# Performance work log

Measured on AMD Instinct MI355X. Metric: run time of the kernel, lower is better.

## Reference

```python
import jax, jax.numpy as jnp
import numpy as np

H = 768        # bert hidden_size
HID = 512      # lstm_hidden
HALF = HID // 2
T = 20         # tagset_size
START, STOP = 18, 19
S = 16386      # input positions incl. CLS/SEP
NEG = -10000.0


def setup_inputs() -> dict:
    key = jax.random.key(0)
    ks = jax.random.split(key, 12)
    sc_x = 1.0
    x = jax.random.normal(ks[0], (1, S, H), dtype=jnp.float32)
    # PyTorch LSTM params (gate order i,f,g,o), one layer, bidirectional
    s_ih = 1.0 / np.sqrt(HALF)
    w_ih_f = jax.random.uniform(ks[1], (4 * HALF, H), jnp.float32, -s_ih, s_ih)
    w_hh_f = jax.random.uniform(ks[2], (4 * HALF, HALF), jnp.float32, -s_ih, s_ih)
    b_ih_f = jax.random.uniform(ks[3], (4 * HALF,), jnp.float32, -s_ih, s_ih)
    b_hh_f = jax.random.uniform(ks[4], (4 * HALF,), jnp.float32, -s_ih, s_ih)
    w_ih_b = jax.random.uniform(ks[5], (4 * HALF, H), jnp.float32, -s_ih, s_ih)
    w_hh_b = jax.random.uniform(ks[6], (4 * HALF, HALF), jnp.float32, -s_ih, s_ih)
    b_ih_b = jax.random.uniform(ks[7], (4 * HALF,), jnp.float32, -s_ih, s_ih)
    b_hh_b = jax.random.uniform(ks[8], (4 * HALF,), jnp.float32, -s_ih, s_ih)
    s_t = 1.0 / np.sqrt(HID)
    w_tag = jax.random.uniform(ks[9], (T, HID), jnp.float32, -s_t, s_t)
    b_tag = jax.random.uniform(ks[10], (T,), jnp.float32, -s_t, s_t)
    transitions = jax.random.normal(ks[11], (T, T), dtype=jnp.float32)
    transitions = transitions.at[START, :].set(NEG).at[:, STOP].set(NEG)
    return {
        "x": x,
        "w_ih_f": w_ih_f, "w_hh_f": w_hh_f, "b_ih_f": b_ih_f, "b_hh_f": b_hh_f,
        "w_ih_b": w_ih_b, "w_hh_b": w_hh_b, "b_ih_b": b_ih_b, "b_hh_b": b_hh_b,
        "w_tag": w_tag, "b_tag": b_tag, "transitions": transitions,
    }


def _lstm_one_step(xt, w_ih, b_ih, b_hh):
    # Original passes [1, N, H] to a batch_first=False LSTM => seq_len=1,
    # batch=N, zero initial state. So each token does ONE cell step:
    # h0=c0=0 => hh contribution is only b_hh.
    g = xt @ w_ih.T + b_ih + b_hh          # [N, 4*HALF]
    i, f, gg, o = jnp.split(g, 4, axis=-1)  # PyTorch gate order i,f,g,o
    c = jax.nn.sigmoid(i) * jnp.tanh(gg)    # f*c0 = 0
    return jax.nn.sigmoid(o) * jnp.tanh(c)  # [N, HALF]


def reference(x, w_ih_f, w_hh_f, b_ih_f, b_hh_f,
              w_ih_b, w_hh_b, b_ih_b, b_hh_b,
              w_tag, b_tag, transitions):
    tok = x[0, 1:-1, :]                     # narrow(1,1,S-2): drop CLS/SEP -> [N,H]
    h_f = _lstm_one_step(tok, w_ih_f, b_ih_f, b_hh_f)
    h_b = _lstm_one_step(tok, w_ih_b, b_ih_b, b_hh_b)
    enc = jnp.concatenate([h_f, h_b], axis=-1)   # [N, HID]
    feats = enc @ w_tag.T + b_tag                # [N, T] emission scores

    # ---- Viterbi decode (sequential DP over tokens) ----
    init = jnp.full((T,), NEG, dtype=feats.dtype).at[START].set(0.0)

    def vstep(fv, feat):
        scores = fv[None, :] + transitions       # [next_tag, prev_tag]
        bp = jnp.argmax(scores, axis=1)          # backpointers [T]
        fv_new = jnp.max(scores, axis=1) + feat
        return fv_new, bp

    fv, bps = jax.lax.scan(vstep, init, feats)   # bps: [N, T]
    terminal = fv + transitions[STOP]
    best = jnp.argmax(terminal)
    path_score = terminal[best]

    def btrack(b, bp):
        return bp[b], b                          # emit tag at time t, move to t-1

    _, best_path = jax.lax.scan(btrack, best, bps, reverse=True)  # [N] in time order
    return path_score, best_path
```

## Files before the change

kernel.cpp:

```cpp
#include <hip/hip_runtime.h>
#include <math.h>

#define HDIM 768
#define HIDD 512
#define NTOK 16384
#define NT 20
#define CHUNKS 128
#define CLEN 128

typedef unsigned short ushort_t;
typedef __attribute__((ext_vector_type(8))) short bf16x8;
typedef __attribute__((ext_vector_type(4))) float f32x4;

__device__ __forceinline__ float sigm(float x){ return 1.0f/(1.0f+expf(-x)); }

__device__ __forceinline__ ushort_t f2bf(float f){
    unsigned int u = __float_as_uint(f);
    unsigned int r = (u + 0x7fffu + ((u >> 16) & 1u)) >> 16;
    return (ushort_t)r;
}
__device__ __forceinline__ float bf2f(ushort_t b){
    return __uint_as_float(((unsigned int)b) << 16);
}

#define GLD16(gp, lp) __builtin_amdgcn_global_load_lds( \
    (const __attribute__((address_space(1))) void*)(gp), \
    (__attribute__((address_space(3))) void*)(lp), 16, 0, 0)

__global__ __launch_bounds__(256) void conv_kernel(
    const float* __restrict__ x,
    const float* __restrict__ wf, const float* __restrict__ wb,
    ushort_t* __restrict__ Ah, ushort_t* __restrict__ Al,
    ushort_t* __restrict__ Bh, ushort_t* __restrict__ Bl)
{
    const int bid = blockIdx.x;
    if (bid < 1152){
        int t = bid*256 + threadIdx.x;
        int n = t / 192, c4 = (t - n*192)*4;
        int dir = n / 768, nr = n - dir*768;
        int gate = nr >> 8, j = nr & 255;
        int wrow = j + ((gate==0)?0:((gate==1)?512:768));
        const float* src = dir ? wb : wf;
        const float4 v = *(const float4*)(src + (size_t)wrow*HDIM + c4);
        float f[4] = {v.x, v.y, v.z, v.w};
        ushort_t h[4], l[4];
        #pragma unroll
        for (int i=0;i<4;++i){
            h[i] = f2bf(f[i]);
            l[i] = f2bf(f[i] - bf2f(h[i]));
        }
        *(ushort4*)(Bh + (size_t)n*HDIM + c4) = make_ushort4(h[0],h[1],h[2],h[3]);
        *(ushort4*)(Bl + (size_t)n*HDIM + c4) = make_ushort4(l[0],l[1],l[2],l[3]);
    } else {
        int t = (bid-1152)*256 + threadIdx.x;
        int row = t / 192, c4 = (t - row*192)*4;
        const float4 v = *(const float4*)(x + (size_t)(row+1)*HDIM + c4);
        float f[4] = {v.x, v.y, v.z, v.w};
        ushort_t h[4], l[4];
        #pragma unroll
        for (int i=0;i<4;++i){
            h[i] = f2bf(f[i]);
            l[i] = f2bf(f[i] - bf2f(h[i]));
        }
        *(ushort4*)(Ah + (size_t)row*HDIM + c4) = make_ushort4(h[0],h[1],h[2],h[3]);
        *(ushort4*)(Al + (size_t)row*HDIM + c4) = make_ushort4(l[0],l[1],l[2],l[3]);
    }
}

__global__ __launch_bounds__(256, 4) void gemm_fused(
    const ushort_t* __restrict__ Ah, const ushort_t* __restrict__ Al,
    const ushort_t* __restrict__ Bh, const ushort_t* __restrict__ Bl,
    const float* __restrict__ bihf, const float* __restrict__ bhhf,
    const float* __restrict__ bihb, const float* __restrict__ bhhb,
    const float* __restrict__ wtag, float* __restrict__ featsp)
{
    __shared__ __align__(16) char smem[32768];
    ushort_t* As_h = (ushort_t*)smem;
    ushort_t* As_l = (ushort_t*)(smem + 4096);
    ushort_t* Bs_h = (ushort_t*)(smem + 8192);
    ushort_t* Bs_l = (ushort_t*)(smem + 16384);
    float* hbuf = (float*)smem;
    float* wts  = (float*)(smem + 16512);

    const int tid = threadIdx.x;
    const int bx = blockIdx.x;
    const int xcd = bx & 7, bidx = bx >> 3;
    const int q = bidx & 3, mt = (bidx >> 2)*8 + xcd;
    const int dir = q >> 1, j0 = (q & 1)*128;
    const int row0 = mt*64;
    const float* __restrict__ bih = dir ? bihb : bihf;
    const float* __restrict__ bhh = dir ? bhhb : bhhf;

    const int lane = tid & 63, wv = tid >> 6;
    const int wm = wv >> 1, wn = wv & 1;
    const int lm = lane & 15, lq = lane >> 4;
    const int wbase = (tid & 192) * 8;

    const int sr = tid >> 2;
    const int k8s = (tid & 3) ^ ((sr & 3) ^ ((sr >> 2) & 3));
    const size_t aoffe = (size_t)(row0 + sr)*HDIM + k8s*8;
    size_t boffe[2];
    #pragma unroll
    for (int g=0; g<2; ++g)
        boffe[g] = (size_t)(g*64 + sr)*HDIM + k8s*8;

    int aoff_lds[2], boff_lds[4];
    #pragma unroll
    for (int f=0; f<2; ++f){
        int m = wm*32 + f*16 + lm;
        int k8p = (lq ^ (m & 3) ^ ((m >> 2) & 3)) & 3;
        aoff_lds[f] = (m*4 + k8p)*8;
    }
    #pragma unroll
    for (int f=0; f<4; ++f){
        int n = wn*64 + f*16 + lm;
        int k8p = (lq ^ (n & 3) ^ ((n >> 2) & 3)) & 3;
        boff_lds[f] = (n*4 + k8p)*8;
    }

    int jcol[4];
    #pragma unroll
    for (int fn=0; fn<4; ++fn) jcol[fn] = j0 + wn*64 + fn*16 + lm;

    float held[2][4][4];
    f32x4 acc[2][4];

    #pragma unroll 1
    for (int p=0; p<3; ++p){
        const size_t bbase = (size_t)(dir*768 + p*256 + j0)*HDIM;

        #pragma unroll
        for (int fm=0; fm<2; ++fm)
            #pragma unroll
            for (int fn=0; fn<4; ++fn)
                acc[fm][fn] = (f32x4){0.f,0.f,0.f,0.f};

        #pragma unroll 1
        for (int kt=0; kt<24; ++kt){
            const int k0 = kt*32;
            GLD16(Ah + aoffe + k0,            &As_h[wbase]);
            GLD16(Al + aoffe + k0,            &As_l[wbase]);
            GLD16(Bh + bbase + boffe[0] + k0, &Bs_h[wbase]);
            GLD16(Bh + bbase + boffe[1] + k0, &Bs_h[2048 + wbase]);
            GLD16(Bl + bbase + boffe[0] + k0, &Bs_l[wbase]);
            GLD16(Bl + bbase + boffe[1] + k0, &Bs_l[2048 + wbase]);
            __syncthreads();
            bf16x8 afh[2], afl[2], bfh[4], bfl[4];
            #pragma unroll
            for (int f=0; f<2; ++f){
                afh[f] = *(const bf16x8*)&As_h[aoff_lds[f]];
                afl[f] = *(const bf16x8*)&As_l[aoff_lds[f]];
            }
            #pragma unroll
            for (int f=0; f<4; ++f){
                bfh[f] = *(const bf16x8*)&Bs_h[boff_lds[f]];
                bfl[f] = *(const bf16x8*)&Bs_l[boff_lds[f]];
            }
            #pragma unroll
            for (int fm=0; fm<2; ++fm)
                #pragma unroll
                for (int fn=0; fn<4; ++fn){
                    acc[fm][fn] = __builtin_amdgcn_mfma_f32_16x16x32_bf16(
                        afh[fm], bfh[fn], acc[fm][fn], 0, 0, 0);
                    acc[fm][fn] = __builtin_amdgcn_mfma_f32_16x16x32_bf16(
                        afl[fm], bfh[fn], acc[fm][fn], 0, 0, 0);
                    acc[fm][fn] = __builtin_amdgcn_mfma_f32_16x16x32_bf16(
                        afh[fm], bfl[fn], acc[fm][fn], 0, 0, 0);
                }
            __syncthreads();
        }

        const int gbase = (p==0) ? 0 : ((p==1) ? 512 : 768);
        float bias[4];
        #pragma unroll
        for (int fn=0; fn<4; ++fn)
            bias[fn] = bih[gbase + jcol[fn]] + bhh[gbase + jcol[fn]];

        if (p==0){
            #pragma unroll
            for (int fm=0; fm<2; ++fm)
                #pragma unroll
                for (int fn=0; fn<4; ++fn)
                    #pragma unroll
                    for (int r=0; r<4; ++r)
                        held[fm][fn][r] = sigm(acc[fm][fn][r] + bias[fn]);
        } else if (p==1){
            #pragma unroll
            for (int fm=0; fm<2; ++fm)
                #pragma unroll
                for (int fn=0; fn<4; ++fn)
                    #pragma unroll
                    for (int r=0; r<4; ++r)
                        held[fm][fn][r] *= tanhf(acc[fm][fn][r] + bias[fn]);
        } else {
            float hv[2][4][4];
            #pragma unroll
            for (int fm=0; fm<2; ++fm)
                #pragma unroll
                for (int fn=0; fn<4; ++fn)
                    #pragma unroll
                    for (int r=0; r<4; ++r)
                        hv[fm][fn][r] = sigm(acc[fm][fn][r] + bias[fn]) * tanhf(held[fm][fn][r]);

            for (int i2=tid; i2<NT*128; i2+=256){
                int t = i2 >> 7, j = i2 & 127;
                wts[i2] = wtag[t*HIDD + dir*256 + j0 + j];
            }
            float* fq = featsp + (size_t)q * (NTOK*NT);
            #pragma unroll 1
            for (int ph=0; ph<2; ++ph){
                __syncthreads();
                if (wm == ph){
                    #pragma unroll
                    for (int fm=0; fm<2; ++fm)
                        #pragma unroll
                        for (int fn=0; fn<4; ++fn)
                            #pragma unroll
                            for (int r=0; r<4; ++r){
                                int mloc = fm*16 + lq*4 + r;
                                int jloc = wn*64 + fn*16 + lm;
                                hbuf[mloc*129 + jloc] = hv[fm][fn][r];
                            }
                }
                __syncthreads();
                const int mrow = tid & 31, grp = tid >> 5;
                if (grp < 5){
                    const int tg0 = grp*4;
                    float s[4] = {0.f,0.f,0.f,0.f};
                    for (int j=0;j<128;++j){
                        float h = hbuf[mrow*129 + j];
                        #pragma unroll
                        for (int tt=0; tt<4; ++tt)
                            s[tt] = fmaf(h, wts[(tg0+tt)*128 + j], s[tt]);
                    }
                    const int mglob = row0 + ph*32 + mrow;
                    #pragma unroll
                    for (int tt=0; tt<4; ++tt)
                        fq[(size_t)mglob*NT + tg0 + tt] = s[tt];
                }
            }
        }
    }
}

__device__ __forceinline__ void load_fl(
    const float* __restrict__ featsp, const float* __restrict__ btg,
    float* fl, int c, int tid, int nthr)
{
    const float4* p0 = (const float4*)(featsp);
    const float4* p1 = (const float4*)(featsp + (size_t)NTOK*NT);
    const float4* p2 = (const float4*)(featsp + (size_t)2*NTOK*NT);
    const float4* p3 = (const float4*)(featsp + (size_t)3*NTOK*NT);
    const int base = c*(CLEN*NT/4);
    for (int idx=tid; idx<CLEN*NT/4; idx+=nthr){
        float4 a = p0[base+idx], b = p1[base+idx];
        float4 d = p2[base+idx], e = p3[base+idx];
        float4 v;
        v.x = (a.x+b.x)+(d.x+e.x);
        v.y = (a.y+b.y)+(d.y+e.y);
        v.z = (a.z+b.z)+(d.z+e.z);
        v.w = (a.w+b.w)+(d.w+e.w);
        int t0 = (idx*4) % 20;
        v.x += btg[t0]; v.y += btg[t0+1]; v.z += btg[t0+2]; v.w += btg[t0+3];
        ((float4*)fl)[idx] = v;
    }
}

__global__ __launch_bounds__(512) void vit_chunkmat(
    const float* __restrict__ featsp, const float* __restrict__ btag,
    const float* __restrict__ trans, float* __restrict__ Pall)
{
    __shared__ float fl[CLEN*NT];
    __shared__ float Pb[2][NT*NT];
    const int c = blockIdx.x, tid = threadIdx.x;
    load_fl(featsp, btag, fl, c, tid, 512);
    const bool act = tid < NT*NT;
    const int i = tid/20, j = tid - i*20;
    float tr[NT];
    if (act){
        #pragma unroll
        for (int k=0;k<NT;++k) tr[k] = trans[i*NT+k];
        Pb[0][tid] = (i==j) ? 0.f : -1e30f;
    }
    __syncthreads();
    int cur = 0;
    for (int t=0;t<CLEN;++t){
        float m = -3.0e38f;
        if (act){
            #pragma unroll
            for (int k=0;k<NT;++k) m = fmaxf(m, tr[k] + Pb[cur][k*NT+j]);
            m += fl[t*NT+i];
            Pb[cur^1][tid] = m;
        }
        __syncthreads();
        cur ^= 1;
    }
    if (act) Pall[(size_t)c*(NT*NT) + tid] = Pb[cur][tid];
}

__global__ __launch_bounds__(128) void vit_scan(
    const float* __restrict__ Pall, const float* __restrict__ trans,
    float* __restrict__ fvstart, float* __restrict__ dout, int* __restrict__ bestws)
{
    __shared__ float Pb[NT*NT];
    __shared__ float fv[NT];
    const int tid = threadIdx.x;
    float4 pn = {0.f,0.f,0.f,0.f};
    if (tid<100) pn = ((const float4*)Pall)[tid];
    if (tid<NT) fv[tid] = (tid==18) ? 0.f : -10000.f;
    for (int c=0;c<CHUNKS;++c){
        if (tid<100) ((float4*)Pb)[tid] = pn;
        if (tid<100 && c+1<CHUNKS) pn = ((const float4*)(Pall + (size_t)(c+1)*(NT*NT)))[tid];
        __syncthreads();
        if (tid<NT) fvstart[c*NT+tid] = fv[tid];
        float nf = -3.0e38f;
        if (tid<NT){
            #pragma unroll
            for (int j=0;j<NT;++j) nf = fmaxf(nf, Pb[tid*NT+j] + fv[j]);
        }
        __syncthreads();
        if (tid<NT) fv[tid] = nf;
    }
    __syncthreads();
    if (tid==0){
        float best = -3.0e38f; int bidx = 0;
        for (int j=0;j<NT;++j){
            float tv = fv[j] + trans[19*NT+j];
            if (tv > best){ best = tv; bidx = j; }
        }
        dout[0] = best;
        bestws[0] = bidx;
    }
}

__global__ __launch_bounds__(64) void vit_replay(
    const float* __restrict__ featsp, const float* __restrict__ btag,
    const float* __restrict__ trans, const float* __restrict__ fvstart,
    unsigned int* __restrict__ bpout, int* __restrict__ Hout)
{
    __shared__ float fl[CLEN*NT];
    __shared__ float fv[NT];
    __shared__ unsigned char bp[CLEN*NT];
    const int c = blockIdx.x, tid = threadIdx.x;
    load_fl(featsp, btag, fl, c, tid, 64);
    float tr[NT];
    if (tid<NT){
        fv[tid] = fvstart[c*NT+tid];
        #pragma unroll
        for (int k=0;k<NT;++k) tr[k] = trans[tid*NT+k];
    }
    __syncthreads();
    for (int t=0;t<CLEN;++t){
        float best = 0.f; int bj = 0;
        if (tid<NT){
            best = tr[0] + fv[0];
            #pragma unroll
            for (int j=1;j<NT;++j){
                float v = tr[j] + fv[j];
                if (v > best){ best = v; bj = j; }
            }
        }
        __syncthreads();
        if (tid<NT){
            fv[tid] = best + fl[t*NT+tid];
            bp[t*NT+tid] = (unsigned char)bj;
        }
        __syncthreads();
    }
    for (int idx=tid; idx<CLEN*NT/4; idx+=64)
        bpout[(size_t)c*(CLEN*NT/4) + idx] = ((unsigned int*)bp)[idx];
    if (tid<NT){
        int m = tid;
        for (int t=CLEN-1;t>=0;--t) m = bp[t*NT+m];
        Hout[c*NT+tid] = m;
    }
}

__global__ __launch_bounds__(64) void bt_fill(
    const unsigned int* __restrict__ bpin, const int* __restrict__ Hin,
    const int* __restrict__ bestws, float* __restrict__ dout)
{
    __shared__ int Hl[CHUNKS*NT];
    __shared__ unsigned char bp[CLEN*NT];
    __shared__ float ob[CLEN];
    const int c = blockIdx.x, tid = threadIdx.x;
    for (int idx=tid; idx<CHUNKS*NT; idx+=64) Hl[idx] = Hin[idx];
    for (int idx=tid; idx<CLEN*NT/4; idx+=64)
        ((unsigned int*)bp)[idx] = bpin[(size_t)c*(CLEN*NT/4) + idx];
    __syncthreads();
    if (tid==0){
        int e = bestws[0];
        for (int cc=CHUNKS-1; cc>c; --cc) e = Hl[cc*NT+e];
        for (int t=CLEN-1;t>=0;--t){ ob[t] = (float)e; e = bp[t*NT+e]; }
    }
    __syncthreads();
    for (int idx=tid; idx<CLEN; idx+=64)
        dout[1 + c*CLEN + idx] = ob[idx];
}

extern "C" void kernel_launch(void* const* d_in, const int* in_sizes, int n_in,
                              void* d_out, int out_size, void* d_ws, size_t ws_size,
                              hipStream_t stream)
{
    const float* x    = (const float*)d_in[0];
    const float* wf   = (const float*)d_in[1];
    const float* bihf = (const float*)d_in[3];
    const float* bhhf = (const float*)d_in[4];
    const float* wb   = (const float*)d_in[5];
    const float* bihb = (const float*)d_in[7];
    const float* bhhb = (const float*)d_in[8];
    const float* wtag = (const float*)d_in[9];
    const float* btag = (const float*)d_in[10];
    const float* trans= (const float*)d_in[11];
    float* out = (float*)d_out;

    char* w = (char*)d_ws;
    ushort_t* Ah = (ushort_t*)w;         w += 25165824;
    ushort_t* Al = (ushort_t*)w;         w += 25165824;
    ushort_t* Bh = (ushort_t*)w;         w += 2359296;
    ushort_t* Bl = (ushort_t*)w;         w += 2359296;
    float* featsp = (float*)w;           w += 5242880;
    float* Pall  = (float*)w;            w += 204800;
    float* fvst  = (float*)w;            w += 10240;
    int* Hmap    = (int*)w;              w += 10240;
    unsigned int* bp = (unsigned int*)w; w += 327680;
    int* best    = (int*)w;

    conv_kernel<<<13440, 256, 0, stream>>>(x, wf, wb, Ah, Al, Bh, Bl);
    gemm_fused<<<1024, 256, 0, stream>>>(Ah, Al, Bh, Bl, bihf, bhhf, bihb, bhhb,
                                         wtag, featsp);
    vit_chunkmat<<<CHUNKS, 512, 0, stream>>>(featsp, btag, trans, Pall);
    vit_scan<<<1, 128, 0, stream>>>(Pall, trans, fvst, out, best);
    vit_replay<<<CHUNKS, 64, 0, stream>>>(featsp, btag, trans, fvst, bp, Hmap);
    bt_fill<<<CHUNKS, 64, 0, stream>>>(bp, Hmap, best, out);
}
```

Baseline: 446.2 us.

## Register-prefetch next GEMM tile instead of direct global-to-LDS loads

```diff
diff --git a/kernel.cpp b/kernel.cpp
--- a/kernel.cpp
+++ b/kernel.cpp
@@ -22,10 +22,6 @@
 __device__ __forceinline__ float bf2f(ushort_t b){
     return __uint_as_float(((unsigned int)b) << 16);
 }
-
-#define GLD16(gp, lp) __builtin_amdgcn_global_load_lds( \
-    (const __attribute__((address_space(1))) void*)(gp), \
-    (__attribute__((address_space(3))) void*)(lp), 16, 0, 0)
 
 __global__ __launch_bounds__(256) void conv_kernel(
     const float* __restrict__ x,
@@ -94,28 +90,26 @@
     const int lane = tid & 63, wv = tid >> 6;
     const int wm = wv >> 1, wn = wv & 1;
     const int lm = lane & 15, lq = lane >> 4;
-    const int wbase = (tid & 192) * 8;
-
-    const int sr = tid >> 2;
-    const int k8s = (tid & 3) ^ ((sr & 3) ^ ((sr >> 2) & 3));
-    const size_t aoffe = (size_t)(row0 + sr)*HDIM + k8s*8;
-    size_t boffe[2];
-    #pragma unroll
-    for (int g=0; g<2; ++g)
-        boffe[g] = (size_t)(g*64 + sr)*HDIM + k8s*8;
+
+    const int srA = tid >> 2;
+    const int ssl = tid & 3;
+    const int gA  = (ssl - srA) & 3;
+    const size_t aoffe = (size_t)(row0 + srA)*HDIM + gA*8;
+    const int srB1 = 64 + srA;
+    const int gB1  = (ssl - srB1) & 3;
+    const size_t boffe0 = (size_t)srB1*HDIM*0 + (size_t)srA*HDIM + gA*8;
+    const size_t boffe1 = (size_t)srB1*HDIM + gB1*8;
 
     int aoff_lds[2], boff_lds[4];
     #pragma unroll
     for (int f=0; f<2; ++f){
         int m = wm*32 + f*16 + lm;
-        int k8p = (lq ^ (m & 3) ^ ((m >> 2) & 3)) & 3;
-        aoff_lds[f] = (m*4 + k8p)*8;
+        aoff_lds[f] = (m*4 + ((lq + m) & 3))*8;
     }
     #pragma unroll
     for (int f=0; f<4; ++f){
         int n = wn*64 + f*16 + lm;
-        int k8p = (lq ^ (n & 3) ^ ((n >> 2) & 3)) & 3;
-        boff_lds[f] = (n*4 + k8p)*8;
+        boff_lds[f] = (n*4 + ((lq + n) & 3))*8;
     }
 
     int jcol[4];
@@ -124,11 +118,20 @@
 
     float held[2][4][4];
     f32x4 acc[2][4];
+    uint4 rAh, rAl, rBh0, rBh1, rBl0, rBl1;
+
+    {
+        const size_t bb = (size_t)(dir*768 + j0)*HDIM;
+        rAh  = *(const uint4*)(Ah + aoffe);
+        rAl  = *(const uint4*)(Al + aoffe);
+        rBh0 = *(const uint4*)(Bh + bb + boffe0);
+        rBh1 = *(const uint4*)(Bh + bb + boffe1);
+        rBl0 = *(const uint4*)(Bl + bb + boffe0);
+        rBl1 = *(const uint4*)(Bl + bb + boffe1);
+    }
 
     #pragma unroll 1
     for (int p=0; p<3; ++p){
-        const size_t bbase = (size_t)(dir*768 + p*256 + j0)*HDIM;
-
         #pragma unroll
         for (int fm=0; fm<2; ++fm)
             #pragma unroll
@@ -137,14 +140,28 @@
 
         #pragma unroll 1
         for (int kt=0; kt<24; ++kt){
-            const int k0 = kt*32;
-            GLD16(Ah + aoffe + k0,            &As_h[wbase]);
-            GLD16(Al + aoffe + k0,            &As_l[wbase]);
-            GLD16(Bh + bbase + boffe[0] + k0, &Bs_h[wbase]);
-            GLD16(Bh + bbase + boffe[1] + k0, &Bs_h[2048 + wbase]);
-            GLD16(Bl + bbase + boffe[0] + k0, &Bs_l[wbase]);
-            GLD16(Bl + bbase + boffe[1] + k0, &Bs_l[2048 + wbase]);
             __syncthreads();
+            *(uint4*)&As_h[(size_t)tid*8]        = rAh;
+            *(uint4*)&As_l[(size_t)tid*8]        = rAl;
+            *(uint4*)&Bs_h[(size_t)tid*8]        = rBh0;
+            *(uint4*)&Bs_h[2048 + (size_t)tid*8] = rBh1;
+            *(uint4*)&Bs_l[(size_t)tid*8]        = rBl0;
+            *(uint4*)&Bs_l[2048 + (size_t)tid*8] = rBl1;
+            __syncthreads();
+
+            int nkt = kt + 1, np = p;
+            if (nkt == 24){ nkt = 0; ++np; }
+            if (np < 3){
+                const int k0 = nkt*32;
+                const size_t bb = (size_t)(dir*768 + np*256 + j0)*HDIM;
+                rAh  = *(const uint4*)(Ah + aoffe + k0);
+                rAl  = *(const uint4*)(Al + aoffe + k0);
+                rBh0 = *(const uint4*)(Bh + bb + boffe0 + k0);
+                rBh1 = *(const uint4*)(Bh + bb + boffe1 + k0);
+                rBl0 = *(const uint4*)(Bl + bb + boffe0 + k0);
+                rBl1 = *(const uint4*)(Bl + bb + boffe1 + k0);
+            }
+
             bf16x8 afh[2], afl[2], bfh[4], bfl[4];
             #pragma unroll
             for (int f=0; f<2; ++f){
@@ -167,7 +184,6 @@
                     acc[fm][fn] = __builtin_amdgcn_mfma_f32_16x16x32_bf16(
                         afh[fm], bfl[fn], acc[fm][fn], 0, 0, 0);
                 }
-            __syncthreads();
         }
 
         const int gbase = (p==0) ? 0 : ((p==1) ? 512 : 768);
@@ -202,6 +218,7 @@
                     for (int r=0; r<4; ++r)
                         hv[fm][fn][r] = sigm(acc[fm][fn][r] + bias[fn]) * tanhf(held[fm][fn][r]);
 
+            __syncthreads();
             for (int i2=tid; i2<NT*128; i2+=256){
                 int t = i2 >> 7, j = i2 & 127;
                 wts[i2] = wtag[t*HIDD + dir*256 + j0 + j];
```

Result: no change. 447.6 us (+0.3%).

## Fuse x bf16 split conversion into GEMM with register prefetch and double-buffered B

Applied to the files above, without the earlier changes.

```diff
diff --git a/kernel.cpp b/kernel.cpp
--- a/kernel.cpp
+++ b/kernel.cpp
@@ -27,58 +27,40 @@
     (const __attribute__((address_space(1))) void*)(gp), \
     (__attribute__((address_space(3))) void*)(lp), 16, 0, 0)
 
+union U8 { ushort_t u[8]; uint4 v; };
+
 __global__ __launch_bounds__(256) void conv_kernel(
+    const float* __restrict__ wf, const float* __restrict__ wb,
+    ushort_t* __restrict__ Bh, ushort_t* __restrict__ Bl)
+{
+    int t = blockIdx.x*256 + threadIdx.x;
+    int n = t / 192, c4 = (t - n*192)*4;
+    int dir = n / 768, nr = n - dir*768;
+    int gate = nr >> 8, j = nr & 255;
+    int wrow = j + ((gate==0)?0:((gate==1)?512:768));
+    const float* src = dir ? wb : wf;
+    const float4 v = *(const float4*)(src + (size_t)wrow*HDIM + c4);
+    float f[4] = {v.x, v.y, v.z, v.w};
+    ushort_t h[4], l[4];
+    #pragma unroll
+    for (int i=0;i<4;++i){
+        h[i] = f2bf(f[i]);
+        l[i] = f2bf(f[i] - bf2f(h[i]));
+    }
+    *(ushort4*)(Bh + (size_t)n*HDIM + c4) = make_ushort4(h[0],h[1],h[2],h[3]);
+    *(ushort4*)(Bl + (size_t)n*HDIM + c4) = make_ushort4(l[0],l[1],l[2],l[3]);
+}
+
+__global__ __launch_bounds__(256, 2) void gemm_fused(
     const float* __restrict__ x,
-    const float* __restrict__ wf, const float* __restrict__ wb,
-    ushort_t* __restrict__ Ah, ushort_t* __restrict__ Al,
-    ushort_t* __restrict__ Bh, ushort_t* __restrict__ Bl)
-{
-    const int bid = blockIdx.x;
-    if (bid < 1152){
-        int t = bid*256 + threadIdx.x;
-        int n = t / 192, c4 = (t - n*192)*4;
-        int dir = n / 768, nr = n - dir*768;
-        int gate = nr >> 8, j = nr & 255;
-        int wrow = j + ((gate==0)?0:((gate==1)?512:768));
-        const float* src = dir ? wb : wf;
-        const float4 v = *(const float4*)(src + (size_t)wrow*HDIM + c4);
-        float f[4] = {v.x, v.y, v.z, v.w};
-        ushort_t h[4], l[4];
-        #pragma unroll
-        for (int i=0;i<4;++i){
-            h[i] = f2bf(f[i]);
-            l[i] = f2bf(f[i] - bf2f(h[i]));
-        }
-        *(ushort4*)(Bh + (size_t)n*HDIM + c4) = make_ushort4(h[0],h[1],h[2],h[3]);
-        *(ushort4*)(Bl + (size_t)n*HDIM + c4) = make_ushort4(l[0],l[1],l[2],l[3]);
-    } else {
-        int t = (bid-1152)*256 + threadIdx.x;
-        int row = t / 192, c4 = (t - row*192)*4;
-        const float4 v = *(const float4*)(x + (size_t)(row+1)*HDIM + c4);
-        float f[4] = {v.x, v.y, v.z, v.w};
-        ushort_t h[4], l[4];
-        #pragma unroll
-        for (int i=0;i<4;++i){
-            h[i] = f2bf(f[i]);
-            l[i] = f2bf(f[i] - bf2f(h[i]));
-        }
-        *(ushort4*)(Ah + (size_t)row*HDIM + c4) = make_ushort4(h[0],h[1],h[2],h[3]);
-        *(ushort4*)(Al + (size_t)row*HDIM + c4) = make_ushort4(l[0],l[1],l[2],l[3]);
-    }
-}
-
-__global__ __launch_bounds__(256, 4) void gemm_fused(
-    const ushort_t* __restrict__ Ah, const ushort_t* __restrict__ Al,
     const ushort_t* __restrict__ Bh, const ushort_t* __restrict__ Bl,
     const float* __restrict__ bihf, const float* __restrict__ bhhf,
     const float* __restrict__ bihb, const float* __restrict__ bhhb,
     const float* __restrict__ wtag, float* __restrict__ featsp)
 {
-    __shared__ __align__(16) char smem[32768];
+    __shared__ __align__(16) char smem[40960];
     ushort_t* As_h = (ushort_t*)smem;
     ushort_t* As_l = (ushort_t*)(smem + 4096);
-    ushort_t* Bs_h = (ushort_t*)(smem + 8192);
-    ushort_t* Bs_l = (ushort_t*)(smem + 16384);
     float* hbuf = (float*)smem;
     float* wts  = (float*)(smem + 16512);
 
@@ -94,28 +76,26 @@
     const int lane = tid & 63, wv = tid >> 6;
     const int wm = wv >> 1, wn = wv & 1;
     const int lm = lane & 15, lq = lane >> 4;
-    const int wbase = (tid & 192) * 8;
-
-    const int sr = tid >> 2;
-    const int k8s = (tid & 3) ^ ((sr & 3) ^ ((sr >> 2) & 3));
-    const size_t aoffe = (size_t)(row0 + sr)*HDIM + k8s*8;
-    size_t boffe[2];
-    #pragma unroll
-    for (int g=0; g<2; ++g)
-        boffe[g] = (size_t)(g*64 + sr)*HDIM + k8s*8;
-
-    int aoff_lds[2], boff_lds[4];
+    const int wb8 = (tid & 192) * 8;
+
+    const int P_ = tid >> 3, s_ = tid & 7;
+    const int q_ = s_ ^ (P_ & 7);
+    const int mA = (P_ << 1) | (q_ >> 2);
+    const int k8s = q_ & 3;
+    const int nB  = mA;
+    const float* aSrc = x + (size_t)(row0 + mA + 1)*HDIM + k8s*8;
+    const int bOff = nB*HDIM + k8s*8;
+
+    int aoff[2], boff[4];
     #pragma unroll
     for (int f=0; f<2; ++f){
         int m = wm*32 + f*16 + lm;
-        int k8p = (lq ^ (m & 3) ^ ((m >> 2) & 3)) & 3;
-        aoff_lds[f] = (m*4 + k8p)*8;
+        aoff[f] = ((m>>1)*8 + ((((m&1)<<2)|lq) ^ ((m>>1)&7)))*8;
     }
     #pragma unroll
     for (int f=0; f<4; ++f){
         int n = wn*64 + f*16 + lm;
-        int k8p = (lq ^ (n & 3) ^ ((n >> 2) & 3)) & 3;
-        boff_lds[f] = (n*4 + k8p)*8;
+        boff[f] = ((n>>1)*8 + ((((n&1)<<2)|lq) ^ ((n>>1)&7)))*8;
     }
 
     int jcol[4];
@@ -124,11 +104,28 @@
 
     float held[2][4][4];
     f32x4 acc[2][4];
+    uint4 rh, rl;
+
+    {
+        const size_t bb = (size_t)(dir*768 + j0)*HDIM;
+        GLD16(Bh + bb + bOff,            smem + 8192  + wb8*2);
+        GLD16(Bh + bb + bOff + 64*HDIM,  smem + 12288 + wb8*2);
+        GLD16(Bl + bb + bOff,            smem + 16384 + wb8*2);
+        GLD16(Bl + bb + bOff + 64*HDIM,  smem + 20480 + wb8*2);
+        float4 ra0 = *(const float4*)(aSrc);
+        float4 ra1 = *(const float4*)(aSrc + 4);
+        float f[8] = {ra0.x,ra0.y,ra0.z,ra0.w,ra1.x,ra1.y,ra1.z,ra1.w};
+        U8 h8, l8;
+        #pragma unroll
+        for (int i=0;i<8;++i){
+            ushort_t h = f2bf(f[i]);
+            h8.u[i] = h; l8.u[i] = f2bf(f[i] - bf2f(h));
+        }
+        rh = h8.v; rl = l8.v;
+    }
 
     #pragma unroll 1
     for (int p=0; p<3; ++p){
-        const size_t bbase = (size_t)(dir*768 + p*256 + j0)*HDIM;
-
         #pragma unroll
         for (int fm=0; fm<2; ++fm)
             #pragma unroll
@@ -137,37 +134,55 @@
 
         #pragma unroll 1
         for (int kt=0; kt<24; ++kt){
-            const int k0 = kt*32;
-            GLD16(Ah + aoffe + k0,            &As_h[wbase]);
-            GLD16(Al + aoffe + k0,            &As_l[wbase]);
-            GLD16(Bh + bbase + boffe[0] + k0, &Bs_h[wbase]);
-            GLD16(Bh + bbase + boffe[1] + k0, &Bs_h[2048 + wbase]);
-            GLD16(Bl + bbase + boffe[0] + k0, &Bs_l[wbase]);
-            GLD16(Bl + bbase + boffe[1] + k0, &Bs_l[2048 + wbase]);
             __syncthreads();
-            bf16x8 afh[2], afl[2], bfh[4], bfl[4];
+            *(uint4*)&As_h[tid*8] = rh;
+            *(uint4*)&As_l[tid*8] = rl;
+            __syncthreads();
+
+            int nkt = kt + 1, np = p;
+            if (nkt == 24){ nkt = 0; ++np; }
+            if (np < 3){
+                const int k0n = nkt*32;
+                const size_t bb = (size_t)(dir*768 + np*256 + j0)*HDIM + k0n;
+                char* bh_d = smem + 8192 + (nkt&1)*16384;
+                GLD16(Bh + bb + bOff,           bh_d + wb8*2);
+                GLD16(Bh + bb + bOff + 64*HDIM, bh_d + 4096 + wb8*2);
+                GLD16(Bl + bb + bOff,           bh_d + 8192 + wb8*2);
+                GLD16(Bl + bb + bOff + 64*HDIM, bh_d + 12288 + wb8*2);
+                float4 ra0 = *(const float4*)(aSrc + k0n);
+                float4 ra1 = *(const float4*)(aSrc + k0n + 4);
+                float f[8] = {ra0.x,ra0.y,ra0.z,ra0.w,ra1.x,ra1.y,ra1.z,ra1.w};
+                U8 h8, l8;
+                #pragma unroll
+                for (int i=0;i<8;++i){
+                    ushort_t h = f2bf(f[i]);
+                    h8.u[i] = h; l8.u[i] = f2bf(f[i] - bf2f(h));
+                }
+                rh = h8.v; rl = l8.v;
+            }
+
+            const ushort_t* Bsh = (const ushort_t*)(smem + 8192 + (kt&1)*16384);
+            const ushort_t* Bsl = (const ushort_t*)(smem + 16384 + (kt&1)*16384);
+            bf16x8 afh[2], afl[2];
             #pragma unroll
             for (int f=0; f<2; ++f){
-                afh[f] = *(const bf16x8*)&As_h[aoff_lds[f]];
-                afl[f] = *(const bf16x8*)&As_l[aoff_lds[f]];
-            }
-            #pragma unroll
-            for (int f=0; f<4; ++f){
-                bfh[f] = *(const bf16x8*)&Bs_h[boff_lds[f]];
-                bfl[f] = *(const bf16x8*)&Bs_l[boff_lds[f]];
-            }
-            #pragma unroll
-            for (int fm=0; fm<2; ++fm)
+                afh[f] = *(const bf16x8*)&As_h[aoff[f]];
+                afl[f] = *(const bf16x8*)&As_l[aoff[f]];
+            }
+            #pragma unroll
+            for (int fn=0; fn<4; ++fn){
+                bf16x8 bh = *(const bf16x8*)&Bsh[boff[fn]];
+                bf16x8 bl = *(const bf16x8*)&Bsl[boff[fn]];
                 #pragma unroll
-                for (int fn=0; fn<4; ++fn){
+                for (int fm=0; fm<2; ++fm){
                     acc[fm][fn] = __builtin_amdgcn_mfma_f32_16x16x32_bf16(
-                        afh[fm], bfh[fn], acc[fm][fn], 0, 0, 0);
+                        afh[fm], bh, acc[fm][fn], 0, 0, 0);
                     acc[fm][fn] = __builtin_amdgcn_mfma_f32_16x16x32_bf16(
-                        afl[fm], bfh[fn], acc[fm][fn], 0, 0, 0);
+                        afl[fm], bh, acc[fm][fn], 0, 0, 0);
                     acc[fm][fn] = __builtin_amdgcn_mfma_f32_16x16x32_bf16(
-                        afh[fm], bfl[fn], acc[fm][fn], 0, 0, 0);
+                        afh[fm], bl, acc[fm][fn], 0, 0, 0);
                 }
-            __syncthreads();
+            }
         }
 
         const int gbase = (p==0) ? 0 : ((p==1) ? 512 : 768);
@@ -202,6 +217,7 @@
                     for (int r=0; r<4; ++r)
                         hv[fm][fn][r] = sigm(acc[fm][fn][r] + bias[fn]) * tanhf(held[fm][fn][r]);
 
+            __syncthreads();
             for (int i2=tid; i2<NT*128; i2+=256){
                 int t = i2 >> 7, j = i2 & 127;
                 wts[i2] = wtag[t*HIDD + dir*256 + j0 + j];
@@ -415,8 +431,6 @@
     float* out = (float*)d_out;
 
     char* w = (char*)d_ws;
-    ushort_t* Ah = (ushort_t*)w;         w += 25165824;
-    ushort_t* Al = (ushort_t*)w;         w += 25165824;
     ushort_t* Bh = (ushort_t*)w;         w += 2359296;
     ushort_t* Bl = (ushort_t*)w;         w += 2359296;
     float* featsp = (float*)w;           w += 5242880;
@@ -426,8 +440,8 @@
     unsigned int* bp = (unsigned int*)w; w += 327680;
     int* best    = (int*)w;
 
-    conv_kernel<<<13440, 256, 0, stream>>>(x, wf, wb, Ah, Al, Bh, Bl);
-    gemm_fused<<<1024, 256, 0, stream>>>(Ah, Al, Bh, Bl, bihf, bhhf, bihb, bhhb,
+    conv_kernel<<<1152, 256, 0, stream>>>(wf, wb, Bh, Bl);
+    gemm_fused<<<1024, 256, 0, stream>>>(x, Bh, Bl, bihf, bhhf, bihb, bhhb,
                                          wtag, featsp);
     vit_chunkmat<<<CHUNKS, 512, 0, stream>>>(featsp, btag, trans, Pall);
     vit_scan<<<1, 128, 0, stream>>>(Pall, trans, fvst, out, best);
```

Measured after the change: 432.6 us. 3.0% less time.
